# Optimization experiments

Measured on AMD Instinct MI355X. Metric: run time of the kernel, lower is better.

The kernel has to match this reference:

```python
import jax, jax.numpy as jnp
import numpy as np

N_NODES = 100000
N_EDGES = 1_600_000
D = 64


def setup_inputs() -> dict:
    key = jax.random.key(0)
    ks = jax.random.split(key, 10)
    features = jax.random.normal(ks[0], (N_NODES, D), dtype=jnp.float32)
    src = jax.random.randint(ks[1], (N_EDGES,), 0, N_NODES, dtype=jnp.int64)
    dst = jax.random.randint(ks[2], (N_EDGES,), 0, N_NODES, dtype=jnp.int64)
    s = 1.0 / np.sqrt(D)
    W0 = jax.random.uniform(ks[3], (D, D), jnp.float32, -s, s)
    b0 = jnp.zeros((D,), jnp.float32)
    W1 = jax.random.uniform(ks[4], (D, D), jnp.float32, -s, s)
    b1 = jnp.zeros((D,), jnp.float32)
    W2 = jax.random.uniform(ks[5], (D, D), jnp.float32, -s, s)
    b2 = jnp.zeros((D,), jnp.float32)
    return {"features": features, "src": src, "dst": dst,
            "W0": W0, "b0": b0, "W1": W1, "b1": b1, "W2": W2, "b2": b2}


def _graph_conv_left(h, src, dst, deg_inv, W, b, act):
    # norm='left': scale source features by 1/out_degree, then copy-sum aggregate
    h = h * deg_inv[:, None]          # [N, d]
    msgs = h[src]                     # [E, d] gather
    agg = jax.ops.segment_sum(msgs, dst, num_segments=N_NODES)  # [N, d]
    out = agg @ W + b
    return act(out) if act is not None else out


def reference(features, src, dst, W0, b0, W1, b1, W2, b2):
    # out-degree with clamp(min=1), as in DGL GraphConv
    deg = jax.ops.segment_sum(jnp.ones((N_EDGES,), jnp.float32), src,
                              num_segments=N_NODES)
    deg_inv = 1.0 / jnp.maximum(deg, 1.0)
    h = _graph_conv_left(features, src, dst, deg_inv, W0, b0, jax.nn.relu)
    h = _graph_conv_left(h, src, dst, deg_inv, W1, b1, jax.nn.relu)
    h = _graph_conv_left(h, src, dst, deg_inv, W2, b2, None)
    mN = jnp.mean(h, axis=0, keepdims=True)  # readout_nodes op='mean', single graph -> [1, d]
    return (h, mN)
```

## Files before the change

### kernel.cpp

```cpp
#include <hip/hip_runtime.h>
#include <hip/hip_fp16.h>

#define D 64
#define NBUK 391
#define CHUNK 8192

__global__ __launch_bounds__(256) void phase1_kernel(const int* __restrict__ src,
                                                     const int* __restrict__ dst,
                                                     int* __restrict__ per_block, int E) {
    __shared__ int h[2 * NBUK];
    int tid = (int)threadIdx.x;
    for (int j = tid; j < 2 * NBUK; j += 256) h[j] = 0;
    __syncthreads();
    int base = blockIdx.x * CHUNK;
    int cnt = min(CHUNK, E - base);
    for (int k = tid * 4; k < cnt; k += 1024) {
        if (k + 3 < cnt) {
            int4 d4 = *(const int4*)(dst + base + k);
            int4 s4 = *(const int4*)(src + base + k);
            atomicAdd(&h[d4.x >> 8], 1); atomicAdd(&h[d4.y >> 8], 1);
            atomicAdd(&h[d4.z >> 8], 1); atomicAdd(&h[d4.w >> 8], 1);
            atomicAdd(&h[NBUK + (s4.x >> 8)], 1); atomicAdd(&h[NBUK + (s4.y >> 8)], 1);
            atomicAdd(&h[NBUK + (s4.z >> 8)], 1); atomicAdd(&h[NBUK + (s4.w >> 8)], 1);
        } else {
            int kend = (k + 4 < cnt) ? k + 4 : cnt;
            for (int t = k; t < kend; ++t) {
                atomicAdd(&h[dst[base + t] >> 8], 1);
                atomicAdd(&h[NBUK + (src[base + t] >> 8)], 1);
            }
        }
    }
    __syncthreads();
    int* pb = per_block + (size_t)blockIdx.x * (2 * NBUK);
    for (int j = tid; j < 2 * NBUK; j += 256) pb[j] = h[j];
}

__global__ __launch_bounds__(64) void scanA_kernel(int* __restrict__ per_block,
                                                   int* __restrict__ total, int nblk) {
    int j = blockIdx.x * 64 + (int)threadIdx.x;
    if (j >= 2 * NBUK) return;
    int pref = 0;
    for (int bk = 0; bk < nblk; ++bk) {
        int idx = bk * (2 * NBUK) + j;
        int v = per_block[idx];
        per_block[idx] = pref;
        pref += v;
    }
    total[j] = pref;
}

__global__ __launch_bounds__(512) void scanB_kernel(const int* __restrict__ total,
                                                    int* __restrict__ cb_dst,
                                                    int* __restrict__ cb_src) {
    __shared__ int s[512];
    int tid = (int)threadIdx.x;
    for (int half = 0; half < 2; ++half) {
        int v = (tid < NBUK) ? total[half * NBUK + tid] : 0;
        s[tid] = v;
        __syncthreads();
        for (int off = 1; off < 512; off <<= 1) {
            int t = (tid >= off) ? s[tid - off] : 0;
            __syncthreads();
            s[tid] += t;
            __syncthreads();
        }
        int* cb = half ? cb_src : cb_dst;
        if (tid < NBUK) cb[tid] = s[tid] - v;
        if (tid == NBUK - 1) cb[NBUK] = s[tid];
        __syncthreads();
    }
}

__global__ __launch_bounds__(256) void phase2_kernel(const int* __restrict__ src,
                                                     const int* __restrict__ dst,
                                                     const int* __restrict__ per_block,
                                                     const int* __restrict__ cb_dst,
                                                     const int* __restrict__ cb_src,
                                                     int* __restrict__ pairs,
                                                     unsigned char* __restrict__ skeys, int E) {
    __shared__ int lcur[2 * NBUK];
    int tid = (int)threadIdx.x;
    const int* pbb = per_block + (size_t)blockIdx.x * (2 * NBUK);
    for (int j = tid; j < 2 * NBUK; j += 256)
        lcur[j] = pbb[j] + (j < NBUK ? cb_dst[j] : cb_src[j - NBUK]);
    __syncthreads();
    int base = blockIdx.x * CHUNK;
    int cnt = min(CHUNK, E - base);
    for (int k = tid * 4; k < cnt; k += 1024) {
        if (k + 3 < cnt) {
            int4 d4 = *(const int4*)(dst + base + k);
            int4 s4 = *(const int4*)(src + base + k);
            int p;
            p = atomicAdd(&lcur[d4.x >> 8], 1); pairs[p] = (s4.x << 8) | (d4.x & 255);
            p = atomicAdd(&lcur[d4.y >> 8], 1); pairs[p] = (s4.y << 8) | (d4.y & 255);
            p = atomicAdd(&lcur[d4.z >> 8], 1); pairs[p] = (s4.z << 8) | (d4.z & 255);
            p = atomicAdd(&lcur[d4.w >> 8], 1); pairs[p] = (s4.w << 8) | (d4.w & 255);
            p = atomicAdd(&lcur[NBUK + (s4.x >> 8)], 1); skeys[p] = (unsigned char)(s4.x & 255);
            p = atomicAdd(&lcur[NBUK + (s4.y >> 8)], 1); skeys[p] = (unsigned char)(s4.y & 255);
            p = atomicAdd(&lcur[NBUK + (s4.z >> 8)], 1); skeys[p] = (unsigned char)(s4.z & 255);
            p = atomicAdd(&lcur[NBUK + (s4.w >> 8)], 1); skeys[p] = (unsigned char)(s4.w & 255);
        } else {
            int kend = (k + 4 < cnt) ? k + 4 : cnt;
            for (int t = k; t < kend; ++t) {
                int dv = dst[base + t], sv = src[base + t];
                int p = atomicAdd(&lcur[dv >> 8], 1);
                pairs[p] = (sv << 8) | (dv & 255);
                p = atomicAdd(&lcur[NBUK + (sv >> 8)], 1);
                skeys[p] = (unsigned char)(sv & 255);
            }
        }
    }
}

__global__ __launch_bounds__(256) void finalize_csr_kernel(const int* __restrict__ pairs,
                                                           const unsigned char* __restrict__ skeys,
                                                           const int* __restrict__ cb_dst,
                                                           const int* __restrict__ cb_src,
                                                           int* __restrict__ row_ptr,
                                                           int* __restrict__ col,
                                                           float* __restrict__ dinv, int N) {
    __shared__ int fine[256];
    __shared__ int lcur[256];
    __shared__ int wtot[4], wexcl[4];
    int b = (int)blockIdx.x;
    int tid = (int)threadIdx.x, lane = tid & 63, wv = tid >> 6;
    int g = b * 256 + tid;

    fine[tid] = 0;
    __syncthreads();
    int sb0 = cb_src[b], sb1 = cb_src[b + 1];
    for (int i = sb0 + tid; i < sb1; i += 256) atomicAdd(&fine[skeys[i]], 1);
    __syncthreads();
    if (g < N) dinv[g] = 1.0f / fmaxf((float)fine[tid], 1.0f);
    __syncthreads();

    fine[tid] = 0;
    __syncthreads();
    int cb0 = cb_dst[b], cb1 = cb_dst[b + 1];
    for (int i = cb0 + tid; i < cb1; i += 256) atomicAdd(&fine[pairs[i] & 255], 1);
    __syncthreads();
    int v = fine[tid], x = v;
#pragma unroll
    for (int d = 1; d < 64; d <<= 1) {
        int t = __shfl_up(x, d);
        if (lane >= d) x += t;
    }
    if (lane == 63) wtot[wv] = x;
    __syncthreads();
    if (tid == 0) {
        int a = 0;
#pragma unroll
        for (int k = 0; k < 4; ++k) { wexcl[k] = a; a += wtot[k]; }
    }
    __syncthreads();
    int excl = x - v + wexcl[wv];
    if (g <= N) row_ptr[g] = cb0 + excl;
    lcur[tid] = cb0 + excl;
    __syncthreads();
    for (int i = cb0 + tid; i < cb1; i += 256) {
        int p = pairs[i];
        int pos = atomicAdd(&lcur[p & 255], 1);
        col[pos] = p >> 8;
    }
}

__global__ __launch_bounds__(256) void prescale_kernel(const float* __restrict__ feat,
                                                       const float* __restrict__ dinv,
                                                       __half* __restrict__ hs, int total8) {
    int i = blockIdx.x * 256 + threadIdx.x;
    if (i >= total8) return;
    int n = i >> 3;
    float sc = dinv[n];
    float4 v0 = ((const float4*)feat)[i * 2];
    float4 v1 = ((const float4*)feat)[i * 2 + 1];
    __half2 h[4];
    h[0] = __floats2half2_rn(v0.x * sc, v0.y * sc);
    h[1] = __floats2half2_rn(v0.z * sc, v0.w * sc);
    h[2] = __floats2half2_rn(v1.x * sc, v1.y * sc);
    h[3] = __floats2half2_rn(v1.z * sc, v1.w * sc);
    *(float4*)(hs + (size_t)i * 8) = *(float4*)h;
}

__device__ inline void accum8(float* a, float4 raw) {
    __half2* h = (__half2*)&raw;
#pragma unroll
    for (int k = 0; k < 4; ++k) {
        float2 f = __half22float2(h[k]);
        a[2 * k] += f.x;
        a[2 * k + 1] += f.y;
    }
}

__global__ __launch_bounds__(256) void fused_kernel(const __half* __restrict__ hs_in,
                                                    const int* __restrict__ row_ptr,
                                                    const int* __restrict__ col,
                                                    const float* __restrict__ W,
                                                    const float* __restrict__ bias,
                                                    const float* __restrict__ dinv,
                                                    float* __restrict__ outf,
                                                    __half* __restrict__ outh,
                                                    float* __restrict__ msum,
                                                    int N, int mode) {
    int tid = (int)threadIdx.x;
    int lane = tid & 63;
    int wv = tid >> 6;
    int sg = lane >> 3;
    int q = lane & 7;
    int g = wv * 8 + sg;

    float Wreg[64];
#pragma unroll
    for (int k = 0; k < 64; ++k) Wreg[k] = W[k * 64 + lane];
    float breg = bias[lane];

    __shared__ float aggT[32][68];
    float colacc = 0.0f;

    int ntiles = (N + 31) >> 5;
    for (int tile = blockIdx.x; tile < ntiles; tile += gridDim.x) {
        int node_g = tile * 32 + g;
        float a[8];
#pragma unroll
        for (int k = 0; k < 8; ++k) a[k] = 0.0f;
        if (node_g < N) {
            int beg = row_ptr[node_g], end = row_ptr[node_g + 1];
            int j = beg;
            for (; j + 3 < end; j += 4) {
                int s0 = col[j], s1 = col[j + 1], s2 = col[j + 2], s3 = col[j + 3];
                float4 r0 = *(const float4*)(hs_in + (size_t)s0 * D + q * 8);
                float4 r1 = *(const float4*)(hs_in + (size_t)s1 * D + q * 8);
                float4 r2 = *(const float4*)(hs_in + (size_t)s2 * D + q * 8);
                float4 r3 = *(const float4*)(hs_in + (size_t)s3 * D + q * 8);
                accum8(a, r0); accum8(a, r1); accum8(a, r2); accum8(a, r3);
            }
            for (; j < end; ++j) {
                int s0 = col[j];
                float4 r0 = *(const float4*)(hs_in + (size_t)s0 * D + q * 8);
                accum8(a, r0);
            }
        }
        *(float4*)(&aggT[g][q * 8]) = make_float4(a[0], a[1], a[2], a[3]);
        *(float4*)(&aggT[g][q * 8 + 4]) = make_float4(a[4], a[5], a[6], a[7]);

#pragma unroll
        for (int rr = 0; rr < 8; ++rr) {
            int r = wv * 8 + rr;
            int node = tile * 32 + r;
            if (node < N) {
                float acc = breg;
                const float4* Ar = (const float4*)(&aggT[r][0]);
#pragma unroll
                for (int k4 = 0; k4 < 16; ++k4) {
                    float4 av = Ar[k4];
                    acc = fmaf(av.x, Wreg[k4 * 4 + 0], acc);
                    acc = fmaf(av.y, Wreg[k4 * 4 + 1], acc);
                    acc = fmaf(av.z, Wreg[k4 * 4 + 2], acc);
                    acc = fmaf(av.w, Wreg[k4 * 4 + 3], acc);
                }
                if (mode == 0) {
                    acc = fmaxf(acc, 0.0f) * dinv[node];
                    outh[(size_t)node * D + lane] = __float2half(acc);
                } else {
                    colacc += acc;
                    outf[(size_t)node * D + lane] = acc;
                }
            }
        }
    }

    if (mode == 1) {
        __shared__ float red[256];
        red[tid] = colacc;
        __syncthreads();
        if (wv == 0) {
            float s = red[lane] + red[64 + lane] + red[128 + lane] + red[192 + lane];
            atomicAdd(&msum[lane], s);
        }
    }
}

__global__ void finalize_kernel(const float* __restrict__ msum, float* __restrict__ outMean,
                                float invN) {
    outMean[threadIdx.x] = msum[threadIdx.x] * invN;
}

extern "C" void kernel_launch(void* const* d_in, const int* in_sizes, int n_in,
                              void* d_out, int out_size, void* d_ws, size_t ws_size,
                              hipStream_t stream) {
    const float* feat = (const float*)d_in[0];
    const int* src = (const int*)d_in[1];
    const int* dst = (const int*)d_in[2];
    const float* W0 = (const float*)d_in[3];
    const float* b0 = (const float*)d_in[4];
    const float* W1 = (const float*)d_in[5];
    const float* b1 = (const float*)d_in[6];
    const float* W2 = (const float*)d_in[7];
    const float* b2 = (const float*)d_in[8];

    const int N = in_sizes[0] / D;
    const int E = in_sizes[1];
    float* out = (float*)d_out;

    const int NBLK = (E + CHUNK - 1) / CHUNK;

    int* wsi = (int*)d_ws;
    const size_t NA = 100352;
    int*   row_ptr  = wsi;
    float* dinv     = (float*)(wsi + NA);
    float* msum     = (float*)(wsi + 2 * NA);
    int*   total    = wsi + 2 * NA + 256;
    int*   cb_dst   = wsi + 2 * NA + 1280;
    int*   cb_src   = wsi + 2 * NA + 1792;
    int*   per_blk  = wsi + 2 * NA + 2304;
    int*   pairs    = wsi + 2 * NA + 155904;
    unsigned char* skeys = (unsigned char*)(pairs + (size_t)E);
    int*   col      = pairs + (size_t)E + 400000;
    __half* hsA     = (__half*)(col + (size_t)E);
    __half* hsB     = hsA + (size_t)N * D;

    hipMemsetAsync(msum, 0, sizeof(float) * D, stream);

    phase1_kernel<<<NBLK, 256, 0, stream>>>(src, dst, per_blk, E);
    scanA_kernel<<<(2 * NBUK + 63) / 64, 64, 0, stream>>>(per_blk, total, NBLK);
    scanB_kernel<<<1, 512, 0, stream>>>(total, cb_dst, cb_src);
    phase2_kernel<<<NBLK, 256, 0, stream>>>(src, dst, per_blk, cb_dst, cb_src, pairs, skeys, E);
    finalize_csr_kernel<<<NBUK, 256, 0, stream>>>(pairs, skeys, cb_dst, cb_src, row_ptr, col, dinv, N);

    prescale_kernel<<<(N * 8 + 255) / 256, 256, 0, stream>>>(feat, dinv, hsA, N * 8);

    const int FG = 1024;
    fused_kernel<<<FG, 256, 0, stream>>>(hsA, row_ptr, col, W0, b0, dinv, nullptr, hsB, msum, N, 0);
    fused_kernel<<<FG, 256, 0, stream>>>(hsB, row_ptr, col, W1, b1, dinv, nullptr, hsA, msum, N, 0);
    fused_kernel<<<FG, 256, 0, stream>>>(hsA, row_ptr, col, W2, b2, dinv, out, nullptr, msum, N, 1);

    finalize_kernel<<<1, 64, 0, stream>>>(msum, out + (size_t)N * D, 1.0f / (float)N);
}
```

Measured before the change: 370.7 us.

## Parallelize bucket scan with transposed per-block layout and one tile per fused block

The per-block histogram is now stored transposed, bucket-major with a fixed stride of 256 blocks, so each wavefront can scan one bucket's counts with int4 loads and shuffle-up prefix sums. This replaces the serial per-column loop over all blocks. The fused aggregation+GEMM kernel now launches one block per 32-node tile instead of a grid-stride loop over 1024 blocks, and its gather loop is unrolled by 8 for more memory-level parallelism. The trade-off is that each block reloads the 64x64 weights into registers, and the fixed stride assumes at most 256 edge chunks.

```diff
diff --git a/kernel.cpp b/kernel.cpp
--- a/kernel.cpp
+++ b/kernel.cpp
@@ -3,14 +3,16 @@
 
 #define D 64
 #define NBUK 391
+#define NBIN (2 * NBUK)
 #define CHUNK 8192
+#define PBSTRIDE 256
 
 __global__ __launch_bounds__(256) void phase1_kernel(const int* __restrict__ src,
                                                      const int* __restrict__ dst,
                                                      int* __restrict__ per_block, int E) {
-    __shared__ int h[2 * NBUK];
+    __shared__ int h[NBIN];
     int tid = (int)threadIdx.x;
-    for (int j = tid; j < 2 * NBUK; j += 256) h[j] = 0;
+    for (int j = tid; j < NBIN; j += 256) h[j] = 0;
     __syncthreads();
     int base = blockIdx.x * CHUNK;
     int cnt = min(CHUNK, E - base);
@@ -31,22 +33,28 @@
         }
     }
     __syncthreads();
-    int* pb = per_block + (size_t)blockIdx.x * (2 * NBUK);
-    for (int j = tid; j < 2 * NBUK; j += 256) pb[j] = h[j];
-}
-
-__global__ __launch_bounds__(64) void scanA_kernel(int* __restrict__ per_block,
-                                                   int* __restrict__ total, int nblk) {
-    int j = blockIdx.x * 64 + (int)threadIdx.x;
-    if (j >= 2 * NBUK) return;
-    int pref = 0;
-    for (int bk = 0; bk < nblk; ++bk) {
-        int idx = bk * (2 * NBUK) + j;
-        int v = per_block[idx];
-        per_block[idx] = pref;
-        pref += v;
-    }
-    total[j] = pref;
+    for (int j = tid; j < NBIN; j += 256) per_block[j * PBSTRIDE + blockIdx.x] = h[j];
+}
+
+__global__ __launch_bounds__(256) void scanA_kernel(int* __restrict__ per_block,
+                                                    int* __restrict__ total) {
+    int wv = (int)threadIdx.x >> 6;
+    int lane = (int)threadIdx.x & 63;
+    int j = blockIdx.x * 4 + wv;
+    if (j >= NBIN) return;
+    int* pb = per_block + (size_t)j * PBSTRIDE;
+    int4 v = *(const int4*)(pb + lane * 4);
+    int s1 = v.x + v.y, s2 = s1 + v.z, s3 = s2 + v.w;
+    int x = s3;
+#pragma unroll
+    for (int d = 1; d < 64; d <<= 1) {
+        int t = __shfl_up(x, d);
+        if (lane >= d) x += t;
+    }
+    int excl = x - s3;
+    int4 r = make_int4(excl, excl + v.x, excl + s1, excl + s2);
+    *(int4*)(pb + lane * 4) = r;
+    if (lane == 63) total[j] = x;
 }
 
 __global__ __launch_bounds__(512) void scanB_kernel(const int* __restrict__ total,
@@ -78,11 +86,11 @@
                                                      const int* __restrict__ cb_src,
                                                      int* __restrict__ pairs,
                                                      unsigned char* __restrict__ skeys, int E) {
-    __shared__ int lcur[2 * NBUK];
+    __shared__ int lcur[NBIN];
     int tid = (int)threadIdx.x;
-    const int* pbb = per_block + (size_t)blockIdx.x * (2 * NBUK);
-    for (int j = tid; j < 2 * NBUK; j += 256)
-        lcur[j] = pbb[j] + (j < NBUK ? cb_dst[j] : cb_src[j - NBUK]);
+    for (int j = tid; j < NBIN; j += 256)
+        lcur[j] = per_block[(size_t)j * PBSTRIDE + blockIdx.x] +
+                  (j < NBUK ? cb_dst[j] : cb_src[j - NBUK]);
     __syncthreads();
     int base = blockIdx.x * CHUNK;
     int cnt = min(CHUNK, E - base);
@@ -214,56 +222,60 @@
     float breg = bias[lane];
 
     __shared__ float aggT[32][68];
+
+    int tile = blockIdx.x;
+    int node_g = tile * 32 + g;
+    float a[8];
+#pragma unroll
+    for (int k = 0; k < 8; ++k) a[k] = 0.0f;
+    if (node_g < N) {
+        int beg = row_ptr[node_g], end = row_ptr[node_g + 1];
+        int j = beg;
+        for (; j + 7 < end; j += 8) {
+            int s0 = col[j], s1 = col[j + 1], s2 = col[j + 2], s3 = col[j + 3];
+            int s4 = col[j + 4], s5 = col[j + 5], s6 = col[j + 6], s7 = col[j + 7];
+            float4 r0 = *(const float4*)(hs_in + (size_t)s0 * D + q * 8);
+            float4 r1 = *(const float4*)(hs_in + (size_t)s1 * D + q * 8);
+            float4 r2 = *(const float4*)(hs_in + (size_t)s2 * D + q * 8);
+            float4 r3 = *(const float4*)(hs_in + (size_t)s3 * D + q * 8);
+            float4 r4 = *(const float4*)(hs_in + (size_t)s4 * D + q * 8);
+            float4 r5 = *(const float4*)(hs_in + (size_t)s5 * D + q * 8);
+            float4 r6 = *(const float4*)(hs_in + (size_t)s6 * D + q * 8);
+            float4 r7 = *(const float4*)(hs_in + (size_t)s7 * D + q * 8);
+            accum8(a, r0); accum8(a, r1); accum8(a, r2); accum8(a, r3);
+            accum8(a, r4); accum8(a, r5); accum8(a, r6); accum8(a, r7);
+        }
+        for (; j < end; ++j) {
+            int s0 = col[j];
+            float4 r0 = *(const float4*)(hs_in + (size_t)s0 * D + q * 8);
+            accum8(a, r0);
+        }
+    }
+    *(float4*)(&aggT[g][q * 8]) = make_float4(a[0], a[1], a[2], a[3]);
+    *(float4*)(&aggT[g][q * 8 + 4]) = make_float4(a[4], a[5], a[6], a[7]);
+
     float colacc = 0.0f;
-
-    int ntiles = (N + 31) >> 5;
-    for (int tile = blockIdx.x; tile < ntiles; tile += gridDim.x) {
-        int node_g = tile * 32 + g;
-        float a[8];
-#pragma unroll
-        for (int k = 0; k < 8; ++k) a[k] = 0.0f;
-        if (node_g < N) {
-            int beg = row_ptr[node_g], end = row_ptr[node_g + 1];
-            int j = beg;
-            for (; j + 3 < end; j += 4) {
-                int s0 = col[j], s1 = col[j + 1], s2 = col[j + 2], s3 = col[j + 3];
-                float4 r0 = *(const float4*)(hs_in + (size_t)s0 * D + q * 8);
-                float4 r1 = *(const float4*)(hs_in + (size_t)s1 * D + q * 8);
-                float4 r2 = *(const float4*)(hs_in + (size_t)s2 * D + q * 8);
-                float4 r3 = *(const float4*)(hs_in + (size_t)s3 * D + q * 8);
-                accum8(a, r0); accum8(a, r1); accum8(a, r2); accum8(a, r3);
+#pragma unroll
+    for (int rr = 0; rr < 8; ++rr) {
+        int r = wv * 8 + rr;
+        int node = tile * 32 + r;
+        if (node < N) {
+            float acc = breg;
+            const float4* Ar = (const float4*)(&aggT[r][0]);
+#pragma unroll
+            for (int k4 = 0; k4 < 16; ++k4) {
+                float4 av = Ar[k4];
+                acc = fmaf(av.x, Wreg[k4 * 4 + 0], acc);
+                acc = fmaf(av.y, Wreg[k4 * 4 + 1], acc);
+                acc = fmaf(av.z, Wreg[k4 * 4 + 2], acc);
+                acc = fmaf(av.w, Wreg[k4 * 4 + 3], acc);
             }
-            for (; j < end; ++j) {
-                int s0 = col[j];
-                float4 r0 = *(const float4*)(hs_in + (size_t)s0 * D + q * 8);
-                accum8(a, r0);
-            }
-        }
-        *(float4*)(&aggT[g][q * 8]) = make_float4(a[0], a[1], a[2], a[3]);
-        *(float4*)(&aggT[g][q * 8 + 4]) = make_float4(a[4], a[5], a[6], a[7]);
-
-#pragma unroll
-        for (int rr = 0; rr < 8; ++rr) {
-            int r = wv * 8 + rr;
-            int node = tile * 32 + r;
-            if (node < N) {
-                float acc = breg;
-                const float4* Ar = (const float4*)(&aggT[r][0]);
-#pragma unroll
-                for (int k4 = 0; k4 < 16; ++k4) {
-                    float4 av = Ar[k4];
-                    acc = fmaf(av.x, Wreg[k4 * 4 + 0], acc);
-                    acc = fmaf(av.y, Wreg[k4 * 4 + 1], acc);
-                    acc = fmaf(av.z, Wreg[k4 * 4 + 2], acc);
-                    acc = fmaf(av.w, Wreg[k4 * 4 + 3], acc);
-                }
-                if (mode == 0) {
-                    acc = fmaxf(acc, 0.0f) * dinv[node];
-                    outh[(size_t)node * D + lane] = __float2half(acc);
-                } else {
-                    colacc += acc;
-                    outf[(size_t)node * D + lane] = acc;
-                }
+            if (mode == 0) {
+                acc = fmaxf(acc, 0.0f) * dinv[node];
+                outh[(size_t)node * D + lane] = __float2half(acc);
+            } else {
+                colacc += acc;
+                outf[(size_t)node * D + lane] = acc;
             }
         }
     }
@@ -312,23 +324,24 @@
     int*   cb_dst   = wsi + 2 * NA + 1280;
     int*   cb_src   = wsi + 2 * NA + 1792;
     int*   per_blk  = wsi + 2 * NA + 2304;
-    int*   pairs    = wsi + 2 * NA + 155904;
+    int*   pairs    = wsi + 2 * NA + 203008;
     unsigned char* skeys = (unsigned char*)(pairs + (size_t)E);
     int*   col      = pairs + (size_t)E + 400000;
     __half* hsA     = (__half*)(col + (size_t)E);
     __half* hsB     = hsA + (size_t)N * D;
 
     hipMemsetAsync(msum, 0, sizeof(float) * D, stream);
+    hipMemsetAsync(per_blk, 0, sizeof(int) * (size_t)NBIN * PBSTRIDE, stream);
 
     phase1_kernel<<<NBLK, 256, 0, stream>>>(src, dst, per_blk, E);
-    scanA_kernel<<<(2 * NBUK + 63) / 64, 64, 0, stream>>>(per_blk, total, NBLK);
+    scanA_kernel<<<(NBIN + 3) / 4, 256, 0, stream>>>(per_blk, total);
     scanB_kernel<<<1, 512, 0, stream>>>(total, cb_dst, cb_src);
     phase2_kernel<<<NBLK, 256, 0, stream>>>(src, dst, per_blk, cb_dst, cb_src, pairs, skeys, E);
     finalize_csr_kernel<<<NBUK, 256, 0, stream>>>(pairs, skeys, cb_dst, cb_src, row_ptr, col, dinv, N);
 
     prescale_kernel<<<(N * 8 + 255) / 256, 256, 0, stream>>>(feat, dinv, hsA, N * 8);
 
-    const int FG = 1024;
+    const int FG = (N + 31) / 32;
     fused_kernel<<<FG, 256, 0, stream>>>(hsA, row_ptr, col, W0, b0, dinv, nullptr, hsB, msum, N, 0);
     fused_kernel<<<FG, 256, 0, stream>>>(hsB, row_ptr, col, W1, b1, dinv, nullptr, hsA, msum, N, 0);
     fused_kernel<<<FG, 256, 0, stream>>>(hsA, row_ptr, col, W2, b2, dinv, out, nullptr, msum, N, 1);
```

Result: slower. 381.6 us (+2.9%).
